# Kernel optimization log

Measured on AMD Instinct MI355X. Metric: run time of the kernel, lower is better.

Reference implementation:

```python
import jax, jax.numpy as jnp
import numpy as np

N, C, T, V = 64, 64, 256, 25
R, O = C // 8, 64  # rel_channels, out_channels
ALPHA = 1.0


def setup_inputs() -> dict:
    key = jax.random.key(0)
    ks = jax.random.split(key, 10)
    s = 0.05
    return {
        "x": jax.random.normal(ks[0], (N, C, T, V), dtype=jnp.float32),
        "A": jax.random.normal(ks[1], (V, V), dtype=jnp.float32),
        "w1": jax.random.normal(ks[2], (R, C), dtype=jnp.float32) * s,
        "b1": jnp.zeros((R,), dtype=jnp.float32),
        "w2": jax.random.normal(ks[3], (R, C), dtype=jnp.float32) * s,
        "b2": jnp.zeros((R,), dtype=jnp.float32),
        "w3": jax.random.normal(ks[4], (O, C), dtype=jnp.float32) * s,
        "b3": jnp.zeros((O,), dtype=jnp.float32),
        "w4": jax.random.normal(ks[5], (O, R), dtype=jnp.float32) * s,
        "b4": jnp.zeros((O,), dtype=jnp.float32),
    }


def reference(x, A, w1, b1, w2, b2, w3, b3, w4, b4):
    # x: (N, C, T, V)
    # conv1/conv2 are 1x1 convs followed by mean over T -> (N, R, V)
    x1 = jnp.einsum('nctv,rc->nrv', x, w1) / x.shape[2] + b1[:, None]
    x2 = jnp.einsum('nctv,rc->nrv', x, w2) / x.shape[2] + b2[:, None]
    # conv3: 1x1 conv -> (N, O, T, V)
    x3 = jnp.einsum('nctv,oc->notv', x, w3) + b3[:, None, None]
    # outer-difference attention over joints: (N, R, V, V)
    att = jnp.tanh(x1[:, :, :, None] - x2[:, :, None, :])
    # conv4 channel mix (R->O), scale, add adjacency: (N, O, V, V)
    m = jnp.einsum('nruv,or->nouv', att, w4) + b4[:, None, None]
    m = m * ALPHA + A[None, None, :, :]
    # aggregation: einsum('ncuv,nctv->nctu')
    out = jnp.einsum('ncuv,nctv->nctu', m, x3)
    return out
```

## Files before the change

### kernel.cpp

```cpp
#include <hip/hip_runtime.h>

#define NN 64
#define CC 64
#define TT 256
#define VV 25
#define RR 8
#define OO 64
#define PLANE 6400
#define SX 201

__global__ __launch_bounds__(256) void k_xsum(const float* __restrict__ x,
                                              float* __restrict__ xsum,
                                              const float* __restrict__ w3,
                                              float* __restrict__ w3t) {
  int nc = blockIdx.x;
  int tid = threadIdx.x;
  if (blockIdx.x < 16) {
    int k = blockIdx.x * 256 + tid;
    int c = k >> 6, o = k & 63;
    w3t[k] = w3[o * 64 + c];
  }
  const float* src = x + (size_t)nc * PLANE;
  __shared__ float s[PLANE + 256];
#pragma unroll
  for (int k = 0; k < 25; ++k) s[k * 256 + tid] = src[k * 256 + tid];
  __syncthreads();
  if (tid < 200) {
    int tg = tid / 25, v = tid - tg * 25;
    float a0 = 0.f, a1 = 0.f, a2 = 0.f, a3 = 0.f;
    for (int k = 0; k < 32; k += 4) {
      a0 += s[(tg + 8 * (k + 0)) * VV + v];
      a1 += s[(tg + 8 * (k + 1)) * VV + v];
      a2 += s[(tg + 8 * (k + 2)) * VV + v];
      a3 += s[(tg + 8 * (k + 3)) * VV + v];
    }
    s[PLANE + tid] = (a0 + a1) + (a2 + a3);
  }
  __syncthreads();
  if (tid < VV) {
    float a = 0.f;
#pragma unroll
    for (int g = 0; g < 8; ++g) a += s[PLANE + g * VV + tid];
    xsum[nc * VV + tid] = a;
  }
}

__global__ __launch_bounds__(256) void k_build_m(
    const float* __restrict__ xsum, const float* __restrict__ A,
    const float* __restrict__ w1, const float* __restrict__ b1,
    const float* __restrict__ w2, const float* __restrict__ b2,
    const float* __restrict__ w4, const float* __restrict__ b4,
    float* __restrict__ mp) {
  int n = blockIdx.x;
  int og = blockIdx.y;
  __shared__ float xs[CC * VV];
  __shared__ float sx1[RR * VV];
  __shared__ float sx2[RR * VV];
  __shared__ float att[RR * 625];
  int tid = threadIdx.x;
  const float* xsn = xsum + n * (CC * VV);
  for (int k = tid; k < CC * VV; k += 256) xs[k] = xsn[k];
  __syncthreads();
  if (tid < RR * VV) {
    int r = tid / VV, v = tid % VV;
    float a1 = 0.f, a2 = 0.f;
#pragma unroll
    for (int c = 0; c < CC; ++c) {
      float xv = xs[c * VV + v];
      a1 = fmaf(w1[r * CC + c], xv, a1);
      a2 = fmaf(w2[r * CC + c], xv, a2);
    }
    sx1[tid] = a1 * (1.f / 256.f) + b1[r];
    sx2[tid] = a2 * (1.f / 256.f) + b2[r];
  }
  __syncthreads();
  for (int k = tid; k < RR * 625; k += 256) {
    int r = k / 625, uv = k % 625;
    int u = uv / VV, v = uv % VV;
    att[k] = tanhf(sx1[r * VV + u] - sx2[r * VV + v]);
  }
  __syncthreads();
  for (int k = tid; k < 16 * 625; k += 256) {
    int o = og * 16 + k / 625, vu = k % 625;
    int v = vu / VV, u = vu % VV;
    float a = b4[o] + A[u * VV + v];
#pragma unroll
    for (int r = 0; r < RR; ++r)
      a = fmaf(w4[o * RR + r], att[r * 625 + u * VV + v], a);
    mp[(((size_t)n * OO + o) * VV + v) * 32 + u] = a;
  }
}

__global__ __launch_bounds__(256, 3) void k_fused(
    const float* __restrict__ x, const float* __restrict__ w3t,
    const float* __restrict__ b3, const float* __restrict__ mp,
    float* __restrict__ out) {
  int n = blockIdx.y;
  int t0 = blockIdx.x * 8;
  __shared__ float s[OO * SX];
  int tid = threadIdx.x;

  if (tid < 200) {
    const float* xp = x + (size_t)n * CC * PLANE + t0 * VV + tid;
    float acc[OO];
#pragma unroll
    for (int o = 0; o < OO; ++o) acc[o] = b3[o];
    for (int c = 0; c < CC; c += 8) {
      float xv[8];
#pragma unroll
      for (int j = 0; j < 8; ++j) xv[j] = xp[(size_t)(c + j) * PLANE];
#pragma unroll
      for (int j = 0; j < 8; ++j) {
        const float* w = w3t + (c + j) * OO;
#pragma unroll
        for (int o = 0; o < OO; ++o) acc[o] = fmaf(w[o], xv[j], acc[o]);
      }
    }
#pragma unroll
    for (int o = 0; o < OO; ++o) s[o * SX + tid] = acc[o];
  }
  __syncthreads();

  {
    int o = tid >> 2, uq = tid & 3;
    const float* mb = mp + (size_t)(n * OO + o) * (VV * 32) + uq * 8;
    const float* xb = s + o * SX;
    float acc[8][8];
#pragma unroll
    for (int t = 0; t < 8; ++t)
#pragma unroll
      for (int j = 0; j < 8; ++j) acc[t][j] = 0.f;
#pragma unroll 2
    for (int v = 0; v < VV; ++v) {
      float4 m0 = *(const float4*)(mb + v * 32);
      float4 m1 = *(const float4*)(mb + v * 32 + 4);
      float xt[8];
#pragma unroll
      for (int t = 0; t < 8; ++t) xt[t] = xb[t * VV + v];
#pragma unroll
      for (int t = 0; t < 8; ++t) {
        acc[t][0] = fmaf(m0.x, xt[t], acc[t][0]);
        acc[t][1] = fmaf(m0.y, xt[t], acc[t][1]);
        acc[t][2] = fmaf(m0.z, xt[t], acc[t][2]);
        acc[t][3] = fmaf(m0.w, xt[t], acc[t][3]);
        acc[t][4] = fmaf(m1.x, xt[t], acc[t][4]);
        acc[t][5] = fmaf(m1.y, xt[t], acc[t][5]);
        acc[t][6] = fmaf(m1.z, xt[t], acc[t][6]);
        acc[t][7] = fmaf(m1.w, xt[t], acc[t][7]);
      }
    }
    __syncthreads();
#pragma unroll
    for (int t = 0; t < 8; ++t)
#pragma unroll
      for (int j = 0; j < 8; ++j) {
        int u = uq * 8 + j;
        if (u < VV) s[o * SX + t * VV + u] = acc[t][j];
      }
  }
  __syncthreads();

  float* ob = out + (size_t)n * OO * PLANE + t0 * VV;
  for (int k = tid; k < OO * 200; k += 256) {
    int oo = k / 200, p = k - oo * 200;
    ob[(size_t)oo * PLANE + p] = s[oo * SX + p];
  }
}

extern "C" void kernel_launch(void* const* d_in, const int* in_sizes, int n_in,
                              void* d_out, int out_size, void* d_ws,
                              size_t ws_size, hipStream_t stream) {
  const float* x = (const float*)d_in[0];
  const float* A = (const float*)d_in[1];
  const float* w1 = (const float*)d_in[2];
  const float* b1 = (const float*)d_in[3];
  const float* w2 = (const float*)d_in[4];
  const float* b2 = (const float*)d_in[5];
  const float* w3 = (const float*)d_in[6];
  const float* b3 = (const float*)d_in[7];
  const float* w4 = (const float*)d_in[8];
  const float* b4 = (const float*)d_in[9];
  float* out = (float*)d_out;
  float* ws = (float*)d_ws;

  float* xsum = ws;
  float* w3t = ws + 102400;
  float* mp = ws + 106496;

  k_xsum<<<NN * CC, 256, 0, stream>>>(x, xsum, w3, w3t);
  k_build_m<<<dim3(NN, 4), 256, 0, stream>>>(xsum, A, w1, b1, w2, b2, w4, b4,
                                             mp);
  k_fused<<<dim3(TT / 8, NN), 256, 0, stream>>>(x, w3t, b3, mp, out);
}
```

Baseline: 317.3 us.

## Halve time tile and split conv across thread halves for higher occupancy

The fused kernel now processes 4 time steps per block instead of 8. The 1x1 conv is split so each half of the block computes 32 of the 64 output channels, which uses all 256 threads and halves the accumulator registers, and launch bounds are raised to allow 6 blocks per CU. The k_xsum load is vectorised with float4, and k_build_m gets twice as many blocks over the output channels. The cost is twice as many fused blocks, each reading x with less reuse and with more per-block overhead.

```diff
diff --git a/kernel.cpp b/kernel.cpp
--- a/kernel.cpp
+++ b/kernel.cpp
@@ -7,7 +7,8 @@
 #define RR 8
 #define OO 64
 #define PLANE 6400
-#define SX 201
+#define SX 101
+
 
 __global__ __launch_bounds__(256) void k_xsum(const float* __restrict__ x,
                                               float* __restrict__ xsum,
@@ -20,10 +21,10 @@
     int c = k >> 6, o = k & 63;
     w3t[k] = w3[o * 64 + c];
   }
-  const float* src = x + (size_t)nc * PLANE;
-  __shared__ float s[PLANE + 256];
-#pragma unroll
-  for (int k = 0; k < 25; ++k) s[k * 256 + tid] = src[k * 256 + tid];
+  const float4* src4 = (const float4*)(x + (size_t)nc * PLANE);
+  __shared__ __align__(16) float s[PLANE + 256];
+  float4* s4 = (float4*)s;
+  for (int k = tid; k < PLANE / 4; k += 256) s4[k] = src4[k];
   __syncthreads();
   if (tid < 200) {
     int tg = tid / 25, v = tid - tg * 25;
@@ -80,8 +81,8 @@
     att[k] = tanhf(sx1[r * VV + u] - sx2[r * VV + v]);
   }
   __syncthreads();
-  for (int k = tid; k < 16 * 625; k += 256) {
-    int o = og * 16 + k / 625, vu = k % 625;
+  for (int k = tid; k < 8 * 625; k += 256) {
+    int o = og * 8 + k / 625, vu = k % 625;
     int v = vu / VV, u = vu % VV;
     float a = b4[o] + A[u * VV + v];
 #pragma unroll
@@ -91,54 +92,66 @@
   }
 }
 
-__global__ __launch_bounds__(256, 3) void k_fused(
+template <int O0>
+__device__ __forceinline__ void conv_half(const float* __restrict__ xb,
+                                          const float* __restrict__ w3t,
+                                          const float* __restrict__ b3,
+                                          float* __restrict__ s) {
+  int p = threadIdx.x & 127;
+  if (p >= 100) return;
+  const float* xp = xb + p;
+  float acc[32];
+#pragma unroll
+  for (int o = 0; o < 32; ++o) acc[o] = b3[O0 + o];
+  for (int c = 0; c < CC; c += 8) {
+    float xv[8];
+#pragma unroll
+    for (int j = 0; j < 8; ++j) xv[j] = xp[(size_t)(c + j) * PLANE];
+#pragma unroll
+    for (int j = 0; j < 8; ++j) {
+      const float* w = w3t + (c + j) * OO + O0;
+#pragma unroll
+      for (int o = 0; o < 32; ++o) acc[o] = fmaf(w[o], xv[j], acc[o]);
+    }
+  }
+#pragma unroll
+  for (int o = 0; o < 32; ++o) s[(O0 + o) * SX + p] = acc[o];
+}
+
+__global__ __launch_bounds__(256, 6) void k_fused(
     const float* __restrict__ x, const float* __restrict__ w3t,
     const float* __restrict__ b3, const float* __restrict__ mp,
     float* __restrict__ out) {
   int n = blockIdx.y;
-  int t0 = blockIdx.x * 8;
+  int t0 = blockIdx.x * 4;
   __shared__ float s[OO * SX];
   int tid = threadIdx.x;
 
-  if (tid < 200) {
-    const float* xp = x + (size_t)n * CC * PLANE + t0 * VV + tid;
-    float acc[OO];
-#pragma unroll
-    for (int o = 0; o < OO; ++o) acc[o] = b3[o];
-    for (int c = 0; c < CC; c += 8) {
-      float xv[8];
-#pragma unroll
-      for (int j = 0; j < 8; ++j) xv[j] = xp[(size_t)(c + j) * PLANE];
-#pragma unroll
-      for (int j = 0; j < 8; ++j) {
-        const float* w = w3t + (c + j) * OO;
-#pragma unroll
-        for (int o = 0; o < OO; ++o) acc[o] = fmaf(w[o], xv[j], acc[o]);
-      }
-    }
-#pragma unroll
-    for (int o = 0; o < OO; ++o) s[o * SX + tid] = acc[o];
-  }
+  const float* xb = x + (size_t)n * CC * PLANE + t0 * VV;
+  if (tid < 128)
+    conv_half<0>(xb, w3t, b3, s);
+  else
+    conv_half<32>(xb, w3t, b3, s);
   __syncthreads();
 
   {
     int o = tid >> 2, uq = tid & 3;
     const float* mb = mp + (size_t)(n * OO + o) * (VV * 32) + uq * 8;
-    const float* xb = s + o * SX;
-    float acc[8][8];
-#pragma unroll
-    for (int t = 0; t < 8; ++t)
+    const float* xr = s + o * SX;
+    float acc[4][8];
+#pragma unroll
+    for (int t = 0; t < 4; ++t)
 #pragma unroll
       for (int j = 0; j < 8; ++j) acc[t][j] = 0.f;
 #pragma unroll 2
     for (int v = 0; v < VV; ++v) {
       float4 m0 = *(const float4*)(mb + v * 32);
       float4 m1 = *(const float4*)(mb + v * 32 + 4);
-      float xt[8];
-#pragma unroll
-      for (int t = 0; t < 8; ++t) xt[t] = xb[t * VV + v];
-#pragma unroll
-      for (int t = 0; t < 8; ++t) {
+      float xt[4];
+#pragma unroll
+      for (int t = 0; t < 4; ++t) xt[t] = xr[t * VV + v];
+#pragma unroll
+      for (int t = 0; t < 4; ++t) {
         acc[t][0] = fmaf(m0.x, xt[t], acc[t][0]);
         acc[t][1] = fmaf(m0.y, xt[t], acc[t][1]);
         acc[t][2] = fmaf(m0.z, xt[t], acc[t][2]);
@@ -151,7 +164,7 @@
     }
     __syncthreads();
 #pragma unroll
-    for (int t = 0; t < 8; ++t)
+    for (int t = 0; t < 4; ++t)
 #pragma unroll
       for (int j = 0; j < 8; ++j) {
         int u = uq * 8 + j;
@@ -161,8 +174,8 @@
   __syncthreads();
 
   float* ob = out + (size_t)n * OO * PLANE + t0 * VV;
-  for (int k = tid; k < OO * 200; k += 256) {
-    int oo = k / 200, p = k - oo * 200;
+  for (int k = tid; k < OO * 100; k += 256) {
+    int oo = k / 100, p = k - oo * 100;
     ob[(size_t)oo * PLANE + p] = s[oo * SX + p];
   }
 }
@@ -188,7 +201,7 @@
   float* mp = ws + 106496;
 
   k_xsum<<<NN * CC, 256, 0, stream>>>(x, xsum, w3, w3t);
-  k_build_m<<<dim3(NN, 4), 256, 0, stream>>>(xsum, A, w1, b1, w2, b2, w4, b4,
+  k_build_m<<<dim3(NN, 8), 256, 0, stream>>>(xsum, A, w1, b1, w2, b2, w4, b4,
                                              mp);
-  k_fused<<<dim3(TT / 8, NN), 256, 0, stream>>>(x, w3t, b3, mp, out);
-}
+  k_fused<<<dim3(TT / 4, NN), 256, 0, stream>>>(x, w3t, b3, mp, out);
+}
```

Measured after the change: 305.0 us. 3.9% less time.
